# Kernel optimization log

Measured on AMD Instinct MI355X. Metric: run time of the kernel, lower is better.

The kernel has to match this reference:

```python
import jax, jax.numpy as jnp
import numpy as np
from jax import lax

FEAT_STRIDE = 16
PRE_NMS_TOPN = 2000
POST_NMS_TOPN = 300
NMS_THRESH = 0.7
MIN_SIZE = 16.0
IMG_H, IMG_W = 1600.0, 2400.0


def _generate_anchors(base_size=16, ratios=(0.5, 1.0, 2.0), scales=(8, 16, 32)):
    w = h = float(base_size)
    xc = yc = 0.5 * (base_size - 1)
    size = w * h
    out = []
    for r in ratios:
        ws = np.round(np.sqrt(size / r))
        hs = np.round(ws * r)
        for s in scales:
            W, H = ws * s, hs * s
            out.append([xc - 0.5 * (W - 1), yc - 0.5 * (H - 1),
                        xc + 0.5 * (W - 1), yc + 0.5 * (H - 1)])
    return np.array(out, dtype=np.float32)  # [9,4]

ANCHORS = jnp.asarray(_generate_anchors())


def _conv(x, w, b, padding):
    y = lax.conv_general_dilated(x, w, (1, 1), padding,
                                 dimension_numbers=('NCHW', 'OIHW', 'NCHW'))
    return y + b[None, :, None, None]


def _nms_mask(boxes, thresh):
    # greedy NMS over score-sorted boxes; returns keep mask
    N = boxes.shape[0]
    x1, y1, x2, y2 = boxes[:, 0], boxes[:, 1], boxes[:, 2], boxes[:, 3]
    areas = (x2 - x1 + 1.0) * (y2 - y1 + 1.0)
    idx = jnp.arange(N)

    def body(i, supp):
        xx1 = jnp.maximum(x1[i], x1)
        yy1 = jnp.maximum(y1[i], y1)
        xx2 = jnp.minimum(x2[i], x2)
        yy2 = jnp.minimum(y2[i], y2)
        w = jnp.maximum(xx2 - xx1 + 1.0, 0.0)
        h = jnp.maximum(yy2 - yy1 + 1.0, 0.0)
        inter = w * h
        iou = inter / (areas[i] + areas - inter)
        cond = (iou > thresh) & (idx > i) & jnp.logical_not(supp[i])
        return supp | cond

    supp = lax.fori_loop(0, N, body, jnp.zeros((N,), dtype=bool))
    return jnp.logical_not(supp)


def reference(features, conv1_w, conv1_b, score_w, score_b, bbox_w, bbox_b, img_info):
    # RPN head
    x = jax.nn.relu(_conv(features, conv1_w, conv1_b, 'SAME'))
    cls = _conv(x, score_w, score_b, 'VALID')    # [1, 2A, H, W]
    deltas = _conv(x, bbox_w, bbox_b, 'VALID')   # [1, 4A, H, W]
    N, C, H, W = cls.shape
    A = C // 2
    # reshape_layer to [N,2,A*H,W], softmax over dim 1, reshape back
    prob = jax.nn.softmax(cls.reshape(N, 2, A * H, W), axis=1).reshape(N, C, H, W)
    fg = prob[:, A:, :, :]                                  # foreground probs
    scores = fg.transpose(0, 2, 3, 1).reshape(-1)           # (H*W*A,)
    d = deltas.transpose(0, 2, 3, 1).reshape(-1, 4)         # (H*W*A, 4)

    # anchor grid (h-major, w-minor, anchor-minor) matching the transpose order
    shift_x = jnp.arange(W, dtype=jnp.float32) * FEAT_STRIDE
    shift_y = jnp.arange(H, dtype=jnp.float32) * FEAT_STRIDE
    sx, sy = jnp.meshgrid(shift_x, shift_y)                 # [H,W]
    shifts = jnp.stack([sx.ravel(), sy.ravel(), sx.ravel(), sy.ravel()], axis=1)
    anchors = (ANCHORS[None, :, :] + shifts[:, None, :]).reshape(-1, 4)

    # bbox_transform_inv decode
    ws = anchors[:, 2] - anchors[:, 0] + 1.0
    hs = anchors[:, 3] - anchors[:, 1] + 1.0
    cx = anchors[:, 0] + 0.5 * ws
    cy = anchors[:, 1] + 0.5 * hs
    pcx = d[:, 0] * ws + cx
    pcy = d[:, 1] * hs + cy
    pw = jnp.exp(d[:, 2]) * ws
    ph = jnp.exp(d[:, 3]) * hs
    props = jnp.stack([pcx - 0.5 * pw, pcy - 0.5 * ph,
                       pcx + 0.5 * pw, pcy + 0.5 * ph], axis=1)
    # clip to image
    props = jnp.stack([jnp.clip(props[:, 0], 0.0, img_info[1] - 1.0),
                       jnp.clip(props[:, 1], 0.0, img_info[0] - 1.0),
                       jnp.clip(props[:, 2], 0.0, img_info[1] - 1.0),
                       jnp.clip(props[:, 3], 0.0, img_info[0] - 1.0)], axis=1)

    # min-size filter (masked, jit-friendly)
    bw = props[:, 2] - props[:, 0] + 1.0
    bh = props[:, 3] - props[:, 1] + 1.0
    min_sz = MIN_SIZE * img_info[2]
    valid = (bw >= min_sz) & (bh >= min_sz)
    scores = jnp.where(valid, scores, -jnp.inf)

    # pre-NMS top-k (sorted desc)
    top_scores, order = lax.top_k(scores, PRE_NMS_TOPN)
    boxes = props[order]
    keep = _nms_mask(boxes, NMS_THRESH)
    kept_scores = jnp.where(keep, top_scores, -jnp.inf)
    post_scores, kidx = lax.top_k(kept_scores, POST_NMS_TOPN)
    final = boxes[kidx]
    rois = jnp.concatenate([jnp.zeros((POST_NMS_TOPN, 1), final.dtype), final], axis=1)
    return rois, post_scores


def setup_inputs() -> dict:
    key = jax.random.key(0)
    ks = jax.random.split(key, 4)
    H, W = 100, 150  # 1600x2400 image at stride 16
    features = jax.random.normal(ks[0], (1, 512, H, W), dtype=jnp.float32)
    conv1_w = jax.random.normal(ks[1], (512, 512, 3, 3), dtype=jnp.float32) * 0.01
    conv1_b = jnp.zeros((512,), dtype=jnp.float32)
    score_w = jax.random.normal(ks[2], (18, 512, 1, 1), dtype=jnp.float32) * 0.01
    score_b = jnp.zeros((18,), dtype=jnp.float32)
    bbox_w = jax.random.normal(ks[3], (36, 512, 1, 1), dtype=jnp.float32) * 0.001
    bbox_b = jnp.zeros((36,), dtype=jnp.float32)
    img_info = jnp.array([IMG_H, IMG_W, 1.0], dtype=jnp.float32)
    return {"features": features, "conv1_w": conv1_w, "conv1_b": conv1_b,
            "score_w": score_w, "score_b": score_b,
            "bbox_w": bbox_w, "bbox_b": bbox_b, "img_info": img_info}
```

## Files before the change

kernel.cpp:

```cpp
#include <hip/hip_runtime.h>
#include <math.h>

#define Hh 100
#define Ww 150
#define Mm 15000
#define NP 135000

typedef double f64x4 __attribute__((ext_vector_type(4)));

#if defined(__HIP_DEVICE_COMPILE__)
#if __has_builtin(__builtin_amdgcn_mfma_f64_16x16x4f64)
#define MFMA64(a,b,c) __builtin_amdgcn_mfma_f64_16x16x4f64((a),(b),(c),0,0,0)
#elif __has_builtin(__builtin_amdgcn_mfma_f64_16x16x4_f64)
#define MFMA64(a,b,c) __builtin_amdgcn_mfma_f64_16x16x4_f64((a),(b),(c),0,0,0)
#else
#error "no f64 mfma builtin on device"
#endif
#else
#define MFMA64(a,b,c) (c)
#endif

__constant__ double ANCH[9][4] = {
  {-84.0,-40.0,99.0,55.0},{-176.0,-88.0,191.0,103.0},{-360.0,-184.0,375.0,191.0},
  {-56.0,-56.0,71.0,71.0},{-120.0,-120.0,135.0,135.0},{-248.0,-248.0,263.0,263.0},
  {-36.0,-80.0,51.0,95.0},{-80.0,-168.0,95.0,183.0},{-168.0,-344.0,183.0,359.0}};

__global__ __launch_bounds__(256) void prep_wT(const float* __restrict__ w,
                                               float* __restrict__ wT) {
  __shared__ float t[32][32][10];
  const int co0 = blockIdx.x * 32, ci0 = blockIdx.y * 32;
  for (int e = threadIdx.x; e < 9216; e += 256) {
    int cr = e / 288;
    int rem = e - cr * 288;
    int cir = rem / 9, tap = rem - cir * 9;
    t[cir][cr][tap] = w[(size_t)(co0 + cr) * 4608 + (ci0 + cir) * 9 + tap];
  }
  __syncthreads();
  for (int e = threadIdx.x; e < 9216; e += 256) {
    int tap = e / 1024;
    int rem = e - tap * 1024;
    int cir = rem >> 5, cr = rem & 31;
    wT[(size_t)tap * 262144 + (size_t)(ci0 + cir) * 512 + (co0 + cr)] = t[cir][cr][tap];
  }
}

__global__ void prep_w54(const float* __restrict__ sw, const float* __restrict__ bw,
                         double* __restrict__ w54) {
  int idx = blockIdx.x * 256 + threadIdx.x;
  if (idx < 54 * 512) {
    int o = idx >> 9, c = idx & 511;
    w54[idx] = (double)((o < 18) ? sw[o * 512 + c] : bw[(o - 18) * 512 + c]);
  }
}

__global__ __launch_bounds__(256, 4) void conv3x3(const float* __restrict__ feat,
                                                  const float* __restrict__ wT,
                                                  const float* __restrict__ bias,
                                                  float* __restrict__ x) {
  __shared__ union {
    struct { float A[32][72]; float B[32][136]; } s;
    float Lx[128][65];
  } sm;
  const int tid = threadIdx.x;
  const int lane = tid & 63;
  const int wv = tid >> 6;
  const int pw = (wv & 1) * 32;
  const int cw = (wv >> 1) * 64;
  const int m0 = blockIdx.x * 64;
  const int n0 = blockIdx.y * 128;
  const int l15 = lane & 15, l4 = lane >> 4;

  f64x4 zero; zero[0] = 0.0; zero[1] = 0.0; zero[2] = 0.0; zero[3] = 0.0;
  f64x4 acc[2][4];
#pragma unroll
  for (int i = 0; i < 2; ++i)
#pragma unroll
    for (int q = 0; q < 4; ++q) acc[i][q] = zero;

  const int pa = tid & 63;
  const int ka = (tid >> 6) * 8;
  const int ma = m0 + pa;
  const int ha = ma / 150, wa = ma - ha * 150;
  const int cq = tid & 31;
  const int kb = (tid >> 5) * 4;

  for (int tap = 0; tap < 9; ++tap) {
    const int dy = tap / 3 - 1, dx = tap - (tap / 3) * 3 - 1;
    const int hh = ha + dy, wwp = wa + dx;
    const bool ok = (ma < Mm) && (hh >= 0) && (hh < Hh) && (wwp >= 0) && (wwp < Ww);
    const int src = hh * Ww + wwp;
    const float* wb = wT + (size_t)tap * 262144 + n0;
    for (int cb = 0; cb < 512; cb += 32) {
#pragma unroll
      for (int kk = 0; kk < 8; ++kk)
        sm.s.A[ka + kk][pa] = ok ? feat[(size_t)(cb + ka + kk) * Mm + src] : 0.0f;
#pragma unroll
      for (int kk = 0; kk < 4; ++kk)
        *(float4*)&sm.s.B[kb + kk][cq * 4] = *(const float4*)&wb[(size_t)(cb + kb + kk) * 512 + cq * 4];
      __syncthreads();
#pragma unroll
      for (int t = 0; t < 8; ++t) {
        const int kt = t * 4 + l4;
        const double a0 = (double)sm.s.A[kt][pw + l15];
        const double a1 = (double)sm.s.A[kt][pw + 16 + l15];
        const double b0 = (double)sm.s.B[kt][cw + l15];
        const double b1 = (double)sm.s.B[kt][cw + 16 + l15];
        const double b2 = (double)sm.s.B[kt][cw + 32 + l15];
        const double b3 = (double)sm.s.B[kt][cw + 48 + l15];
        acc[0][0] = MFMA64(a0, b0, acc[0][0]);
        acc[0][1] = MFMA64(a0, b1, acc[0][1]);
        acc[0][2] = MFMA64(a0, b2, acc[0][2]);
        acc[0][3] = MFMA64(a0, b3, acc[0][3]);
        acc[1][0] = MFMA64(a1, b0, acc[1][0]);
        acc[1][1] = MFMA64(a1, b1, acc[1][1]);
        acc[1][2] = MFMA64(a1, b2, acc[1][2]);
        acc[1][3] = MFMA64(a1, b3, acc[1][3]);
      }
      __syncthreads();
    }
  }

  const double ap1 = (l4 == 0) ? (double)l15 : 0.0;
  const double bp1 = (l4 == 0) ? 1.0 : 0.0;
  const f64x4 rowp = MFMA64(ap1, bp1, zero);
  const double ap2 = (l4 == 0) ? 1.0 : 0.0;
  const double bp2 = (l4 == 0) ? (double)l15 : 0.0;
  const f64x4 colp = MFMA64(ap2, bp2, zero);

#pragma unroll
  for (int i = 0; i < 2; ++i)
#pragma unroll
    for (int q = 0; q < 4; ++q)
#pragma unroll
      for (int r = 0; r < 4; ++r) {
        const int row = pw + i * 16 + (int)rowp[r];
        const int col = cw + q * 16 + (int)colp[r];
        const double v = acc[i][q][r] + (double)bias[n0 + col];
        sm.Lx[col][row] = (float)(v > 0.0 ? v : 0.0);
      }
  __syncthreads();
  for (int e = tid; e < 64 * 128; e += 256) {
    const int co = e >> 6, p = e & 63;
    const int m = m0 + p;
    if (m < Mm) x[(size_t)(n0 + co) * Mm + m] = sm.Lx[co][p];
  }
}

__global__ __launch_bounds__(256) void conv1x1(const float* __restrict__ x,
                                               const double* __restrict__ w54,
                                               const float* __restrict__ sb,
                                               const float* __restrict__ bb,
                                               float* __restrict__ cls,
                                               float* __restrict__ dl) {
  int m = blockIdx.x * 256 + threadIdx.x;
  int g = blockIdx.y;
  double acc[9];
#pragma unroll
  for (int o = 0; o < 9; ++o) acc[o] = 0.0;
  if (m < Mm) {
    const double* wg = w54 + (size_t)g * 9 * 512;
    for (int c = 0; c < 512; ++c) {
      double v = (double)x[(size_t)c * Mm + m];
#pragma unroll
      for (int o = 0; o < 9; ++o) acc[o] += v * wg[o * 512 + c];
    }
#pragma unroll
    for (int o = 0; o < 9; ++o) {
      int oo = g * 9 + o;
      if (oo < 18) cls[oo * Mm + m] = (float)(acc[o] + (double)sb[oo]);
      else dl[(oo - 18) * Mm + m] = (float)(acc[o] + (double)bb[oo - 18]);
    }
  }
}

__global__ void decode(const float* __restrict__ cls, const float* __restrict__ dl,
                       const float* __restrict__ info, double4* __restrict__ props,
                       float* __restrict__ scoresF, unsigned long long* __restrict__ keys64,
                       unsigned* __restrict__ keys32, unsigned* __restrict__ hist) {
  int i = blockIdx.x * 256 + threadIdx.x;
  if (i >= NP) return;
  int m = i / 9, a = i - m * 9;
  int h = m / 150, w = m - h * 150;
  double c0 = (double)cls[a * Mm + m], c1 = (double)cls[(9 + a) * Mm + m];
  double mx = fmax(c0, c1);
  double e0 = exp(c0 - mx), e1 = exp(c1 - mx);
  double p = e1 / (e0 + e1);
  double d0 = (double)dl[(a * 4 + 0) * Mm + m], d1 = (double)dl[(a * 4 + 1) * Mm + m];
  double d2 = (double)dl[(a * 4 + 2) * Mm + m], d3 = (double)dl[(a * 4 + 3) * Mm + m];
  double sx = (double)w * 16.0, sy = (double)h * 16.0;
  double ax1 = ANCH[a][0] + sx, ay1 = ANCH[a][1] + sy;
  double ax2 = ANCH[a][2] + sx, ay2 = ANCH[a][3] + sy;
  double aw = ax2 - ax1 + 1.0, ah = ay2 - ay1 + 1.0;
  double cx = ax1 + 0.5 * aw, cy = ay1 + 0.5 * ah;
  double pcx = d0 * aw + cx, pcy = d1 * ah + cy;
  double pw = exp(d2) * aw, ph = exp(d3) * ah;
  double x1 = pcx - 0.5 * pw, y1 = pcy - 0.5 * ph;
  double x2 = pcx + 0.5 * pw, y2 = pcy + 0.5 * ph;
  double IH = (double)info[0], IW = (double)info[1], sc = (double)info[2];
  x1 = fmin(fmax(x1, 0.0), IW - 1.0); y1 = fmin(fmax(y1, 0.0), IH - 1.0);
  x2 = fmin(fmax(x2, 0.0), IW - 1.0); y2 = fmin(fmax(y2, 0.0), IH - 1.0);
  double bwd = x2 - x1 + 1.0, bhd = y2 - y1 + 1.0;
  bool valid = (bwd >= 16.0 * sc) && (bhd >= 16.0 * sc);
  double score = valid ? p : -__builtin_inf();
  double4 pr; pr.x = x1; pr.y = y1; pr.z = x2; pr.w = y2;
  props[i] = pr;
  float pf = (float)score;
  scoresF[i] = pf;
  unsigned long long b = (unsigned long long)__double_as_longlong(score);
  unsigned long long s = (b >> 63) ? ~b : (b | 0x8000000000000000ull);
  unsigned long long k = ~s;
  keys64[i] = (k & ~0x3FFFFull) | (unsigned long long)i;
  unsigned ub = __float_as_uint(pf);
  unsigned us = (ub >> 31) ? ~ub : (ub | 0x80000000u);
  unsigned k32 = ~us;
  keys32[i] = k32;
  atomicAdd(&hist[k32 >> 16], 1u);
}

__global__ __launch_bounds__(1024) void cutoff_k(const unsigned* __restrict__ hist,
                                                 int* __restrict__ Bout) {
  __shared__ unsigned ps[1024];
  int t = threadIdx.x;
  unsigned s = 0;
  for (int b = t * 64; b < t * 64 + 64; ++b) s += hist[b];
  ps[t] = s; __syncthreads();
  for (int off = 1; off < 1024; off <<= 1) {
    unsigned a = ps[t];
    unsigned bb2 = (t >= off) ? ps[t - off] : 0u;
    __syncthreads();
    ps[t] = a + bb2;
    __syncthreads();
  }
  unsigned excl = ps[t] - s;
  if (excl < 2000u) {
    unsigned run = excl;
    for (int b = t * 64; b < t * 64 + 64; ++b) {
      unsigned nb = run + hist[b];
      if (run < 2000u && nb >= 2000u) *Bout = b;
      run = nb;
    }
  }
}

__global__ void compact_k(const unsigned* __restrict__ keys32,
                          const unsigned long long* __restrict__ keys64,
                          const int* __restrict__ Bptr,
                          unsigned long long* __restrict__ cand, int* __restrict__ cnt) {
  int i = blockIdx.x * 256 + threadIdx.x;
  if (i >= NP) return;
  int B = *Bptr;
  if ((int)(keys32[i] >> 16) <= B) {
    int pos = atomicAdd(cnt, 1);
    if (pos < 8192) cand[pos] = keys64[i];
  }
}

__global__ __launch_bounds__(1024) void sort_top(const unsigned long long* __restrict__ cand,
                                                 const int* __restrict__ pcnt,
                                                 const double4* __restrict__ props,
                                                 const float* __restrict__ scoresF,
                                                 double4* __restrict__ boxes2000,
                                                 float* __restrict__ score2000) {
  __shared__ unsigned long long sh[8192];
  int t = threadIdx.x;
  int cnt = *pcnt; if (cnt > 8192) cnt = 8192;
  for (int i = t; i < 8192; i += 1024) sh[i] = (i < cnt) ? cand[i] : ~0ull;
  __syncthreads();
  for (int kb = 1; kb <= 13; ++kb) {
    int k = 1 << kb;
    for (int jb = kb - 1; jb >= 0; --jb) {
      int j = 1 << jb;
      for (int s = t; s < 4096; s += 1024) {
        int i = ((s >> jb) << (jb + 1)) | (s & (j - 1));
        int l = i + j;
        bool up = ((i & k) == 0);
        unsigned long long a = sh[i], b = sh[l];
        if (up ? (a > b) : (a < b)) { sh[i] = b; sh[l] = a; }
      }
      __syncthreads();
    }
  }
  for (int r = t; r < 2000; r += 1024) {
    unsigned long long key = sh[r];
    int idx = (int)(key & 0x3FFFFull);
    boxes2000[r] = props[idx];
    score2000[r] = scoresF[idx];
  }
}

__global__ __launch_bounds__(256) void nms_mask(const double4* __restrict__ boxes,
                                                unsigned long long* __restrict__ mask) {
  int tid = threadIdx.x;
  int r = blockIdx.x * 8 + (tid >> 5);
  int wd = tid & 31;
  double4 bi = boxes[r];
  double ai = (bi.z - bi.x + 1.0) * (bi.w - bi.y + 1.0);
  unsigned long long bits = 0;
  int j0 = wd * 64;
  int jmax = 2000 - j0; if (jmax > 64) jmax = 64;
  for (int jj = 0; jj < jmax; ++jj) {
    int j = j0 + jj;
    if (j > r) {
      double4 bj = boxes[j];
      double xx1 = fmax(bi.x, bj.x), yy1 = fmax(bi.y, bj.y);
      double xx2 = fmin(bi.z, bj.z), yy2 = fmin(bi.w, bj.w);
      double w_ = fmax(xx2 - xx1 + 1.0, 0.0), h_ = fmax(yy2 - yy1 + 1.0, 0.0);
      double inter = w_ * h_;
      double aj = (bj.z - bj.x + 1.0) * (bj.w - bj.y + 1.0);
      double iou = inter / (ai + aj - inter);
      if (iou > 0.7) bits |= 1ull << jj;
    }
  }
  mask[r * 32 + wd] = bits;
}

__global__ __launch_bounds__(256) void suppress(const unsigned long long* __restrict__ mask,
                                                unsigned long long* __restrict__ aliveOut) {
  __shared__ unsigned long long rows[64][32];
  int tid = threadIdx.x;
  int lane = tid & 63;
  unsigned long long myword = 0;
  if (tid < 64) {
    if (lane < 31) myword = ~0ull;
    else if (lane == 31) myword = 0xFFFFull;
  }
  for (int c = 0; c < 32; ++c) {
    __syncthreads();
    for (int idx = tid; idx < 2048; idx += 256) {
      int g = c * 2048 + idx;
      ((unsigned long long*)rows)[idx] = (g < 64000) ? mask[g] : 0ull;
    }
    __syncthreads();
    if (tid < 64) {
      for (int r = 0; r < 64; ++r) {
        int i = c * 64 + r;
        unsigned long long rw = rows[r][lane & 31];
        unsigned long long aw = __shfl(myword, i >> 6);
        if ((aw >> (i & 63)) & 1ull) {
          if (lane < 32) myword &= ~rw;
        }
      }
    }
  }
  __syncthreads();
  if (tid < 32) aliveOut[tid] = myword;
}

__global__ __launch_bounds__(1024) void finalize(const unsigned long long* __restrict__ alive,
                                                 const double4* __restrict__ boxes,
                                                 const float* __restrict__ scores,
                                                 float* __restrict__ out) {
  __shared__ int ps[1024];
  int t = threadIdx.x;
  int e0 = 2 * t, e1 = 2 * t + 1;
  int f0 = (e0 < 2000) ? (int)((alive[e0 >> 6] >> (e0 & 63)) & 1ull) : 0;
  int f1 = (e1 < 2000) ? (int)((alive[e1 >> 6] >> (e1 & 63)) & 1ull) : 0;
  int v = f0 + f1;
  ps[t] = v; __syncthreads();
  for (int off = 1; off < 1024; off <<= 1) {
    int a = ps[t];
    int b = (t >= off) ? ps[t - off] : 0;
    __syncthreads();
    ps[t] = a + b;
    __syncthreads();
  }
  int incl = ps[t];
  int excl = incl - v;
  int Na = ps[1023];
  if (f0 && excl < 300) {
    double4 bx = boxes[e0];
    out[excl * 5 + 0] = 0.f; out[excl * 5 + 1] = (float)bx.x; out[excl * 5 + 2] = (float)bx.y;
    out[excl * 5 + 3] = (float)bx.z; out[excl * 5 + 4] = (float)bx.w;
    out[1500 + excl] = scores[e0];
  }
  int p1 = excl + f0;
  if (f1 && p1 < 300) {
    double4 bx = boxes[e1];
    out[p1 * 5 + 0] = 0.f; out[p1 * 5 + 1] = (float)bx.x; out[p1 * 5 + 2] = (float)bx.y;
    out[p1 * 5 + 3] = (float)bx.z; out[p1 * 5 + 4] = (float)bx.w;
    out[1500 + p1] = scores[e1];
  }
  if (Na < 300) {
    if (e0 < 2000 && !f0) {
      int q = Na + (e0 - excl);
      if (q < 300) {
        double4 bx = boxes[e0];
        out[q * 5 + 0] = 0.f; out[q * 5 + 1] = (float)bx.x; out[q * 5 + 2] = (float)bx.y;
        out[q * 5 + 3] = (float)bx.z; out[q * 5 + 4] = (float)bx.w;
        out[1500 + q] = -__builtin_inff();
      }
    }
    if (e1 < 2000 && !f1) {
      int q = Na + (e1 - (excl + f0));
      if (q < 300) {
        double4 bx = boxes[e1];
        out[q * 5 + 0] = 0.f; out[q * 5 + 1] = (float)bx.x; out[q * 5 + 2] = (float)bx.y;
        out[q * 5 + 3] = (float)bx.z; out[q * 5 + 4] = (float)bx.w;
        out[1500 + q] = -__builtin_inff();
      }
    }
  }
}

extern "C" void kernel_launch(void* const* d_in, const int* in_sizes, int n_in,
                              void* d_out, int out_size, void* d_ws, size_t ws_size,
                              hipStream_t stream) {
  (void)in_sizes; (void)n_in; (void)out_size; (void)ws_size;
  const float* feat = (const float*)d_in[0];
  const float* w1   = (const float*)d_in[1];
  const float* b1   = (const float*)d_in[2];
  const float* sw   = (const float*)d_in[3];
  const float* sb   = (const float*)d_in[4];
  const float* bw   = (const float*)d_in[5];
  const float* bb   = (const float*)d_in[6];
  const float* info = (const float*)d_in[7];
  float* out = (float*)d_out;

  char* ws = (char*)d_ws;
  size_t off = 0;
  auto alloc = [&](size_t bytes) -> void* {
    void* p = ws + off;
    off += (bytes + 255) & ~(size_t)255;
    return p;
  };
  float* x        = (float*)alloc((size_t)512 * Mm * 4);
  float* wT       = (float*)alloc((size_t)9 * 512 * 512 * 4);
  double* w54     = (double*)alloc((size_t)54 * 512 * 8);
  float* cls      = (float*)alloc((size_t)18 * Mm * 4);
  float* dl       = (float*)alloc((size_t)36 * Mm * 4);
  double4* props  = (double4*)alloc((size_t)NP * 32);
  float* scoresF  = (float*)alloc((size_t)NP * 4);
  unsigned long long* keys64 = (unsigned long long*)alloc((size_t)NP * 8);
  unsigned* keys32 = (unsigned*)alloc((size_t)NP * 4);
  unsigned* hist   = (unsigned*)alloc((size_t)65536 * 4);
  int* Bptr        = (int*)alloc(256);
  int* cnt         = (int*)alloc(256);
  unsigned long long* cand = (unsigned long long*)alloc((size_t)8192 * 8);
  double4* boxes2000 = (double4*)alloc((size_t)2000 * 32);
  float* score2000   = (float*)alloc((size_t)2000 * 4);
  unsigned long long* mask  = (unsigned long long*)alloc((size_t)2000 * 32 * 8);
  unsigned long long* alive = (unsigned long long*)alloc((size_t)32 * 8);

  hipMemsetAsync(hist, 0, 65536 * 4, stream);
  hipMemsetAsync(cnt, 0, 4, stream);

  prep_wT<<<dim3(16, 16), 256, 0, stream>>>(w1, wT);
  prep_w54<<<108, 256, 0, stream>>>(sw, bw, w54);
  conv3x3<<<dim3(235, 4), 256, 0, stream>>>(feat, wT, b1, x);
  conv1x1<<<dim3(59, 6), 256, 0, stream>>>(x, w54, sb, bb, cls, dl);
  decode<<<528, 256, 0, stream>>>(cls, dl, info, props, scoresF, keys64, keys32, hist);
  cutoff_k<<<1, 1024, 0, stream>>>(hist, Bptr);
  compact_k<<<528, 256, 0, stream>>>(keys32, keys64, Bptr, cand, cnt);
  sort_top<<<1, 1024, 0, stream>>>(cand, cnt, props, scoresF, boxes2000, score2000);
  nms_mask<<<250, 256, 0, stream>>>(boxes2000, mask);
  suppress<<<1, 256, 0, stream>>>(mask, alive);
  finalize<<<1, 1024, 0, stream>>>(alive, boxes2000, score2000, out);
}
```

Measured before the change: 1.840 ms.

## Double-buffer conv3x3 tiles with direct global-to-LDS loads

Flattens the tap and channel-block loops into one chunk loop and double-buffers the A and B shared-memory tiles. Each next chunk is loaded with global_load_lds while the current one feeds the f64 MFMAs, and zero padding comes from a small zeroed buffer. This removes the register staging of loads and one barrier per chunk. In exchange, LDS per block roughly doubles, which can lower occupancy, and correctness relies on load completion being enforced at the barrier.

```diff
diff --git a/kernel.cpp b/kernel.cpp
--- a/kernel.cpp
+++ b/kernel.cpp
@@ -16,8 +16,12 @@
 #else
 #error "no f64 mfma builtin on device"
 #endif
+#define GLOAD4(g,l) __builtin_amdgcn_global_load_lds( \
+    (const __attribute__((address_space(1))) unsigned*)(g), \
+    (__attribute__((address_space(3))) unsigned*)(l), 4, 0, 0)
 #else
 #define MFMA64(a,b,c) (c)
+#define GLOAD4(g,l) ((void)(g),(void)(l))
 #endif
 
 __constant__ double ANCH[9][4] = {
@@ -56,9 +60,10 @@
 __global__ __launch_bounds__(256, 4) void conv3x3(const float* __restrict__ feat,
                                                   const float* __restrict__ wT,
                                                   const float* __restrict__ bias,
+                                                  const float* __restrict__ zp,
                                                   float* __restrict__ x) {
   __shared__ union {
-    struct { float A[32][72]; float B[32][136]; } s;
+    struct { float A[2][32][72]; float B[2][32][136]; } s;
     float Lx[128][65];
   } sm;
   const int tid = threadIdx.x;
@@ -77,47 +82,55 @@
 #pragma unroll
     for (int q = 0; q < 4; ++q) acc[i][q] = zero;
 
-  const int pa = tid & 63;
-  const int ka = (tid >> 6) * 8;
-  const int ma = m0 + pa;
+  const int ka = wv * 8;
+  const int ma = m0 + lane;
   const int ha = ma / 150, wa = ma - ha * 150;
-  const int cq = tid & 31;
-  const int kb = (tid >> 5) * 4;
-
-  for (int tap = 0; tap < 9; ++tap) {
-    const int dy = tap / 3 - 1, dx = tap - (tap / 3) * 3 - 1;
+
+  auto stage = [&](int cn, int buf) {
+    const int tap = cn >> 4;
+    const int cb = (cn & 15) << 5;
+    const int t3 = tap / 3;
+    const int dy = t3 - 1, dx = tap - t3 * 3 - 1;
     const int hh = ha + dy, wwp = wa + dx;
     const bool ok = (ma < Mm) && (hh >= 0) && (hh < Hh) && (wwp >= 0) && (wwp < Ww);
-    const int src = hh * Ww + wwp;
-    const float* wb = wT + (size_t)tap * 262144 + n0;
-    for (int cb = 0; cb < 512; cb += 32) {
-#pragma unroll
-      for (int kk = 0; kk < 8; ++kk)
-        sm.s.A[ka + kk][pa] = ok ? feat[(size_t)(cb + ka + kk) * Mm + src] : 0.0f;
-#pragma unroll
-      for (int kk = 0; kk < 4; ++kk)
-        *(float4*)&sm.s.B[kb + kk][cq * 4] = *(const float4*)&wb[(size_t)(cb + kb + kk) * 512 + cq * 4];
-      __syncthreads();
-#pragma unroll
-      for (int t = 0; t < 8; ++t) {
-        const int kt = t * 4 + l4;
-        const double a0 = (double)sm.s.A[kt][pw + l15];
-        const double a1 = (double)sm.s.A[kt][pw + 16 + l15];
-        const double b0 = (double)sm.s.B[kt][cw + l15];
-        const double b1 = (double)sm.s.B[kt][cw + 16 + l15];
-        const double b2 = (double)sm.s.B[kt][cw + 32 + l15];
-        const double b3 = (double)sm.s.B[kt][cw + 48 + l15];
-        acc[0][0] = MFMA64(a0, b0, acc[0][0]);
-        acc[0][1] = MFMA64(a0, b1, acc[0][1]);
-        acc[0][2] = MFMA64(a0, b2, acc[0][2]);
-        acc[0][3] = MFMA64(a0, b3, acc[0][3]);
-        acc[1][0] = MFMA64(a1, b0, acc[1][0]);
-        acc[1][1] = MFMA64(a1, b1, acc[1][1]);
-        acc[1][2] = MFMA64(a1, b2, acc[1][2]);
-        acc[1][3] = MFMA64(a1, b3, acc[1][3]);
-      }
-      __syncthreads();
-    }
+    const int src = ok ? (hh * Ww + wwp) : 0;
+    const float* ab = feat + (size_t)(cb + ka) * Mm + src;
+#pragma unroll
+    for (int kk = 0; kk < 8; ++kk)
+      GLOAD4(ok ? (ab + (size_t)kk * Mm) : zp, &sm.s.A[buf][ka + kk][0]);
+    const float* wbase = wT + (size_t)tap * 262144 + (size_t)(cb + ka) * 512 + n0 + lane;
+#pragma unroll
+    for (int kk = 0; kk < 8; ++kk) {
+      GLOAD4(wbase + (size_t)kk * 512,      &sm.s.B[buf][ka + kk][0]);
+      GLOAD4(wbase + (size_t)kk * 512 + 64, &sm.s.B[buf][ka + kk][64]);
+    }
+  };
+
+  stage(0, 0);
+  __syncthreads();
+
+  for (int c = 0; c < 144; ++c) {
+    const int b = c & 1;
+    if (c + 1 < 144) stage(c + 1, b ^ 1);
+#pragma unroll
+    for (int t = 0; t < 8; ++t) {
+      const int kt = t * 4 + l4;
+      const double a0 = (double)sm.s.A[b][kt][pw + l15];
+      const double a1 = (double)sm.s.A[b][kt][pw + 16 + l15];
+      const double b0 = (double)sm.s.B[b][kt][cw + l15];
+      const double b1 = (double)sm.s.B[b][kt][cw + 16 + l15];
+      const double b2 = (double)sm.s.B[b][kt][cw + 32 + l15];
+      const double b3 = (double)sm.s.B[b][kt][cw + 48 + l15];
+      acc[0][0] = MFMA64(a0, b0, acc[0][0]);
+      acc[0][1] = MFMA64(a0, b1, acc[0][1]);
+      acc[0][2] = MFMA64(a0, b2, acc[0][2]);
+      acc[0][3] = MFMA64(a0, b3, acc[0][3]);
+      acc[1][0] = MFMA64(a1, b0, acc[1][0]);
+      acc[1][1] = MFMA64(a1, b1, acc[1][1]);
+      acc[1][2] = MFMA64(a1, b2, acc[1][2]);
+      acc[1][3] = MFMA64(a1, b3, acc[1][3]);
+    }
+    __syncthreads();
   }
 
   const double ap1 = (l4 == 0) ? (double)l15 : 0.0;
@@ -440,13 +453,15 @@
   float* score2000   = (float*)alloc((size_t)2000 * 4);
   unsigned long long* mask  = (unsigned long long*)alloc((size_t)2000 * 32 * 8);
   unsigned long long* alive = (unsigned long long*)alloc((size_t)32 * 8);
+  float* zp        = (float*)alloc(256);
 
   hipMemsetAsync(hist, 0, 65536 * 4, stream);
   hipMemsetAsync(cnt, 0, 4, stream);
+  hipMemsetAsync(zp, 0, 256, stream);
 
   prep_wT<<<dim3(16, 16), 256, 0, stream>>>(w1, wT);
   prep_w54<<<108, 256, 0, stream>>>(sw, bw, w54);
-  conv3x3<<<dim3(235, 4), 256, 0, stream>>>(feat, wT, b1, x);
+  conv3x3<<<dim3(235, 4), 256, 0, stream>>>(feat, wT, b1, zp, x);
   conv1x1<<<dim3(59, 6), 256, 0, stream>>>(x, w54, sb, bb, cls, dl);
   decode<<<528, 256, 0, stream>>>(cls, dl, info, props, scoresF, keys64, keys32, hist);
   cutoff_k<<<1, 1024, 0, stream>>>(hist, Bptr);
```

Result: slower. 2.033 ms (+10.5%).
